# Optimization experiments

Hardware: AMD Instinct MI355X
Metric: run time of the kernel (lower is better)

## Reference

```python
import jax, jax.numpy as jnp
import numpy as np

B = 512
SHAPE = (64, 64, 64)   # mode dims I1,I2,I3
RANKS = (8, 8, 8)      # Tucker ranks R1,R2,R3
SEP = 4                # separation rank (number of Tucker terms)


def setup_inputs() -> dict:
    key = jax.random.key(0)
    k_x, k_core, k_fac = jax.random.split(key, 3)
    x = jax.random.normal(k_x, (B,) + SHAPE, dtype=jnp.float32)
    core = jax.random.normal(k_core, RANKS, dtype=jnp.float32)
    # factors[s, k] is the mode-k factor matrix [I_k, R_k] of term s
    factors = jax.random.normal(k_fac, (SEP, len(SHAPE), SHAPE[0], RANKS[0]), dtype=jnp.float32)
    return {"x": x, "core": core, "factors": factors}


def reference(x, core, factors):
    # expand_to_tensor: sum_s multi_mode_dot(core, factors[s])
    # T[i,j,k] = sum_s sum_abc core[a,b,c] * U1_s[i,a] * U2_s[j,b] * U3_s[k,c]
    T = jnp.einsum('abc,sia,sjb,skc->ijk',
                   core, factors[:, 0], factors[:, 1], factors[:, 2])
    # tenalg.inner(x, T, n_modes=order): contract the last `order` modes -> [B]
    return jnp.einsum('bijk,ijk->b', x, T)
```

## Files before the change

### kernel.cpp

```cpp
#include <hip/hip_runtime.h>
#include <hip/hip_bf16.h>


__global__ __launch_bounds__(256) void tucker_expand_kernel(
    const float* __restrict__ core,
    const float* __restrict__ factors,
    float* __restrict__ T) {
  const int i = blockIdx.x;
  const int t = threadIdx.x;

  __shared__ float core_s[512];
  __shared__ float c1[64];
  __shared__ float c2[512];
  __shared__ float u3[64 * 9];

  core_s[t]       = core[t];
  core_s[t + 256] = core[t + 256];

  float tacc[16];
#pragma unroll
  for (int m = 0; m < 16; ++m) tacc[m] = 0.f;

  for (int s = 0; s < 4; ++s) {
    {
      const float* U3 = factors + ((s * 3 + 2) * 64) * 8;
      int e0 = t, e1 = t + 256;
      u3[(e0 >> 3) * 9 + (e0 & 7)] = U3[e0];
      u3[(e1 >> 3) * 9 + (e1 & 7)] = U3[e1];
    }
    __syncthreads();

    if (t < 64) {
      const float* U1row = factors + ((s * 3 + 0) * 64 + i) * 8;
      float v = 0.f;
#pragma unroll
      for (int a = 0; a < 8; ++a) v += core_s[a * 64 + t] * U1row[a];
      c1[t] = v;
    }
    __syncthreads();

    {
      const float* U2 = factors + ((s * 3 + 1) * 64) * 8;
#pragma unroll
      for (int rep = 0; rep < 2; ++rep) {
        int e = t + rep * 256;
        int j = e >> 3, c = e & 7;
        float v = 0.f;
#pragma unroll
        for (int b = 0; b < 8; ++b) v += U2[j * 8 + b] * c1[b * 8 + c];
        c2[e] = v;
      }
    }
    __syncthreads();

#pragma unroll
    for (int m = 0; m < 16; ++m) {
      int e = m * 256 + t;
      int j = e >> 6, k = e & 63;
      float v = 0.f;
#pragma unroll
      for (int c = 0; c < 8; ++c) v += u3[k * 9 + c] * c2[j * 8 + c];
      tacc[m] += v;
    }
    __syncthreads();
  }

#pragma unroll
  for (int m = 0; m < 16; ++m) T[i * 4096 + m * 256 + t] = tacc[m];
}

__global__ __launch_bounds__(256) void dot_partial_kernel(
    const float* __restrict__ x,
    const float* __restrict__ T,
    float* __restrict__ partials) {
  const int blk = blockIdx.x;
  const int b = blk & 511;
  const int chunk = blk >> 9;
  const int t = threadIdx.x;

  const float4* x4 = reinterpret_cast<const float4*>(
      x + (size_t)b * 262144 + (size_t)chunk * 32768);
  const float4* t4 = reinterpret_cast<const float4*>(T + (size_t)chunk * 32768);

  float a0 = 0.f, a1 = 0.f, a2 = 0.f, a3 = 0.f;
#pragma unroll 4
  for (int i = 0; i < 32; ++i) {
    int idx = i * 256 + t;
    float4 xv = x4[idx];
    float4 tv = t4[idx];
    a0 += xv.x * tv.x;
    a1 += xv.y * tv.y;
    a2 += xv.z * tv.z;
    a3 += xv.w * tv.w;
  }
  float sum = (a0 + a1) + (a2 + a3);

#pragma unroll
  for (int off = 32; off > 0; off >>= 1) sum += __shfl_down(sum, off, 64);

  __shared__ float wsum[4];
  int wave = t >> 6, lane = t & 63;
  if (lane == 0) wsum[wave] = sum;
  __syncthreads();
  if (t == 0) {
    partials[(size_t)chunk * 512 + b] = (wsum[0] + wsum[1]) + (wsum[2] + wsum[3]);
  }
}

__global__ void reduce_kernel(const float* __restrict__ partials,
                              float* __restrict__ out) {
  int b = blockIdx.x * blockDim.x + threadIdx.x;
  if (b < 512) {
    float s = 0.f;
#pragma unroll
    for (int c = 0; c < 8; ++c) s += partials[c * 512 + b];
    out[b] = s;
  }
}

extern "C" void kernel_launch(void* const* d_in, const int* in_sizes, int n_in,
                              void* d_out, int out_size, void* d_ws, size_t ws_size,
                              hipStream_t stream) {
  const float* x       = (const float*)d_in[0];
  const float* core    = (const float*)d_in[1];
  const float* factors = (const float*)d_in[2];
  float* out = (float*)d_out;

  float* T        = (float*)d_ws;
  float* partials = T + 262144;

  tucker_expand_kernel<<<64, 256, 0, stream>>>(core, factors, T);
  dot_partial_kernel<<<4096, 256, 0, stream>>>(x, T, partials);
  reduce_kernel<<<1, 512, 0, stream>>>(partials, out);
}
```

Baseline: 681.1 us.

## Replace reduce kernel with atomics, reorder blocks by batch, use nontemporal x loads

Drops the third reduce kernel: the expand kernel zeroes the output and each dot block atomically adds its partial sum into out[b]. Block indexing now walks the 8 chunks of one batch element consecutively, so adjacent blocks read contiguous memory. The x stream uses nontemporal loads to avoid polluting cache, and the loop unroll goes from 4 to 8. Float atomics make the summation order nondeterministic, and removing one launch saves only a few microseconds on a kernel bound by HBM bandwidth.

```diff
diff --git a/kernel.cpp b/kernel.cpp
--- a/kernel.cpp
+++ b/kernel.cpp
@@ -2,12 +2,20 @@
 #include <hip/hip_bf16.h>
 
 
+typedef float fvec4 __attribute__((ext_vector_type(4)));
+
 __global__ __launch_bounds__(256) void tucker_expand_kernel(
     const float* __restrict__ core,
     const float* __restrict__ factors,
-    float* __restrict__ T) {
+    float* __restrict__ T,
+    float* __restrict__ out) {
   const int i = blockIdx.x;
   const int t = threadIdx.x;
+
+  if (i == 0) {
+    out[t] = 0.f;
+    out[t + 256] = 0.f;
+  }
 
   __shared__ float core_s[512];
   __shared__ float c1[64];
@@ -72,22 +80,22 @@
 __global__ __launch_bounds__(256) void dot_partial_kernel(
     const float* __restrict__ x,
     const float* __restrict__ T,
-    float* __restrict__ partials) {
+    float* __restrict__ out) {
   const int blk = blockIdx.x;
-  const int b = blk & 511;
-  const int chunk = blk >> 9;
+  const int chunk = blk & 7;
+  const int b = blk >> 3;
   const int t = threadIdx.x;
 
-  const float4* x4 = reinterpret_cast<const float4*>(
+  const fvec4* x4 = reinterpret_cast<const fvec4*>(
       x + (size_t)b * 262144 + (size_t)chunk * 32768);
-  const float4* t4 = reinterpret_cast<const float4*>(T + (size_t)chunk * 32768);
+  const fvec4* t4 = reinterpret_cast<const fvec4*>(T + (size_t)chunk * 32768);
 
   float a0 = 0.f, a1 = 0.f, a2 = 0.f, a3 = 0.f;
-#pragma unroll 4
+#pragma unroll 8
   for (int i = 0; i < 32; ++i) {
     int idx = i * 256 + t;
-    float4 xv = x4[idx];
-    float4 tv = t4[idx];
+    fvec4 xv = __builtin_nontemporal_load(x4 + idx);
+    fvec4 tv = t4[idx];
     a0 += xv.x * tv.x;
     a1 += xv.y * tv.y;
     a2 += xv.z * tv.z;
@@ -103,18 +111,7 @@
   if (lane == 0) wsum[wave] = sum;
   __syncthreads();
   if (t == 0) {
-    partials[(size_t)chunk * 512 + b] = (wsum[0] + wsum[1]) + (wsum[2] + wsum[3]);
-  }
-}
-
-__global__ void reduce_kernel(const float* __restrict__ partials,
-                              float* __restrict__ out) {
-  int b = blockIdx.x * blockDim.x + threadIdx.x;
-  if (b < 512) {
-    float s = 0.f;
-#pragma unroll
-    for (int c = 0; c < 8; ++c) s += partials[c * 512 + b];
-    out[b] = s;
+    atomicAdd(&out[b], (wsum[0] + wsum[1]) + (wsum[2] + wsum[3]));
   }
 }
 
@@ -126,10 +123,8 @@
   const float* factors = (const float*)d_in[2];
   float* out = (float*)d_out;
 
-  float* T        = (float*)d_ws;
-  float* partials = T + 262144;
+  float* T = (float*)d_ws;
 
-  tucker_expand_kernel<<<64, 256, 0, stream>>>(core, factors, T);
-  dot_partial_kernel<<<4096, 256, 0, stream>>>(x, T, partials);
-  reduce_kernel<<<1, 512, 0, stream>>>(partials, out);
+  tucker_expand_kernel<<<64, 256, 0, stream>>>(core, factors, T, out);
+  dot_partial_kernel<<<4096, 256, 0, stream>>>(x, T, out);
 }
```

New measurement: 669.0 us. About the same (-1.8%).
